# Kernel tuning notes

Measured on AMD Instinct MI355X. Metric: run time of the kernel, lower is better.

## Reference

```python
import jax, jax.numpy as jnp
import numpy as np

B, T, N, K = 8, 256, 128, 64
EPS = 1e-12  # torch.nn.functional.normalize clamp


def setup_inputs() -> dict:
    key = jax.random.key(0)
    ks = jax.random.split(key, 6)
    observation = jax.random.normal(ks[0], (B, T, K), dtype=jnp.float32)
    duration = jax.random.randint(ks[1], (B,), 1, T + 1)  # in [1, T]
    # time-varying transition matrices, strictly positive (probabilities pre-normalization)
    transition = jax.random.uniform(ks[2], (T, B, N, N), dtype=jnp.float32, minval=0.05, maxval=1.0)
    start_prob = jax.random.uniform(ks[3], (B, N), dtype=jnp.float32, minval=0.05, maxval=1.0)
    W_emit = jax.random.normal(ks[4], (K, N), dtype=jnp.float32) * 0.05
    b_emit = jnp.zeros((N,), dtype=jnp.float32)
    return {"observation": observation, "duration": duration, "transition": transition,
            "start_prob": start_prob, "W_emit": W_emit, "b_emit": b_emit}


def _log_emission(observation, W_emit, b_emit):
    # emission module: linear K->N then log-softmax over states -> [B,T,N]
    logits = jnp.einsum('btk,kn->btn', observation, W_emit) + b_emit
    return jax.nn.log_softmax(logits, axis=-1)


def reference(observation, duration, transition, start_prob, W_emit, b_emit):
    log_emit = _log_emission(observation, W_emit, b_emit)            # [B,T,N]
    # L1-normalize transitions along target dim (dim=2 of [B,N,N]) then log
    l1 = jnp.clip(jnp.sum(jnp.abs(transition), axis=-1, keepdims=True), EPS)
    logT = jnp.log(transition / l1)                                  # [T,B,N,N]

    la0 = log_emit[:, 0, :] + jnp.log(start_prob)                    # [B,N]

    def step(la_prev, xs):
        le_t, lT_t = xs                                              # [B,N], [B,N,N]
        # log-domain matmul: out[b,j] = logsumexp_k la_prev[b,k] + logT[b,k,j]
        la = le_t + jax.nn.logsumexp(la_prev[:, :, None] + lT_t, axis=1)
        return la, la

    le_seq = jnp.swapaxes(log_emit, 0, 1)                            # [T,B,N]
    _, alphas = jax.lax.scan(step, la0, (le_seq[1:], logT[1:]))      # [T-1,B,N]
    log_alpha = jnp.concatenate([la0[:, None, :], jnp.swapaxes(alphas, 0, 1)], axis=1)  # [B,T,N]

    log_sums = jax.nn.logsumexp(log_alpha, axis=2)                   # [B,T]
    log_probs = jnp.take_along_axis(log_sums, (duration - 1)[:, None], axis=1)  # [B,1]
    return log_probs
```

## Files before the change

### kernel.cpp

```cpp
#include <hip/hip_runtime.h>
#include <math.h>
#include <stdint.h>

#define B_ 8
#define T_ 256
#define N_ 128
#define K_ 64
#define NCH 32
#define LOG128 4.852030263919617f
#define STRIDE_S 4128

typedef __attribute__((ext_vector_type(2))) unsigned int u32x2;
typedef __attribute__((ext_vector_type(4))) unsigned int u32x4;
typedef __attribute__((ext_vector_type(4))) float f32x4;
typedef __attribute__((ext_vector_type(8))) short short8;

__device__ __forceinline__ uint32_t cvtpk(float lo, float hi) {
    uint32_t r;
    asm("v_cvt_pk_bf16_f32 %0, %1, %2" : "=v"(r) : "v"(lo), "v"(hi));
    return r;
}
__device__ __forceinline__ float blo(uint32_t w) { return __uint_as_float(w << 16); }
__device__ __forceinline__ float bhi(uint32_t w) { return __uint_as_float(w & 0xffff0000u); }

#define TRRD(dst, addr) asm volatile("ds_read_b64_tr_b16 %0, %1" : "=v"(dst) : "v"(addr) : "memory")
#define WAITL8  { asm volatile("s_waitcnt lgkmcnt(8)"  ::: "memory"); __builtin_amdgcn_sched_barrier(0); }
#define WAITL0  { asm volatile("s_waitcnt lgkmcnt(0)"  ::: "memory"); __builtin_amdgcn_sched_barrier(0); }

__global__ __launch_bounds__(128) void k_emit(
    const float* __restrict__ obs,
    const int*   __restrict__ dur,
    const float* __restrict__ W,
    const float* __restrict__ bias,
    float* __restrict__ e)
{
    int bt = blockIdx.x;
    int b  = bt >> 8;
    int t  = bt & 255;
    if (t >= dur[b]) return;
    int n = threadIdx.x;
    __shared__ float o[K_];
    __shared__ float wmax[2];
    __shared__ float wsum[2];
    if (n < K_) o[n] = obs[(size_t)bt * K_ + n];
    __syncthreads();
    float acc = bias[n];
    #pragma unroll
    for (int k = 0; k < K_; ++k)
        acc = fmaf(o[k], W[k * N_ + n], acc);
    float m = acc;
    #pragma unroll
    for (int off = 32; off; off >>= 1) m = fmaxf(m, __shfl_xor(m, off));
    int w = n >> 6;
    if ((n & 63) == 0) wmax[w] = m;
    __syncthreads();
    float M = fmaxf(wmax[0], wmax[1]);
    float ex = expf(acc - M);
    float s = ex;
    #pragma unroll
    for (int off = 32; off; off >>= 1) s += __shfl_xor(s, off);
    if ((n & 63) == 0) wsum[w] = s;
    __syncthreads();
    float S = wsum[0] + wsum[1];
    e[(size_t)bt * N_ + n] = ex / S;
}

__global__ __launch_bounds__(512, 1) void k_chunk(
    const float* __restrict__ trans,
    const int*   __restrict__ dur,
    const float* __restrict__ e,
    uint32_t* __restrict__ gout)
{
    const int bc = blockIdx.x;
    const int b  = bc & 7;
    const int c  = bc >> 3;
    const int d  = dur[b];
    const int t0 = c * 8 + 1;
    if (t0 > d - 1) return;
    int te = c * 8 + 8; if (te > d - 1) te = d - 1;

    const int tid  = threadIdx.x;
    const int lane = tid & 63;
    const int wv   = tid >> 6;
    const int cc   = lane & 15;
    const int gq   = lane >> 4;

    __shared__ __align__(16) uint8_t ldsC[2][8 * STRIDE_S];
    __shared__ __align__(16) uint8_t strips[8 * STRIDE_S];

    {
        uint32_t* sw = (uint32_t*)(strips + wv * STRIDE_S);
        #pragma unroll
        for (int i = 0; i < 16; ++i) sw[lane + i * 64] = 0;
        if (lane < 16)
            ((uint16_t*)(strips + wv * STRIDE_S))[(16 * wv + lane) * 16 + lane] = 0x3F80u;
    }

    const uint32_t sbase = (uint32_t)(uintptr_t)&strips[wv * STRIDE_S];
    const uint32_t lt    = (uint32_t)(cc * 2 + gq * 256);
    const int row0 = tid >> 5;
    const int jbp  = (tid & 31) >> 2;
    const int cc0  = (tid & 3) << 2;

    f32x4 acc[8];

    float4 v[8];
    float  ev[8];
    {
        const float4* gp = (const float4*)(trans + (((size_t)t0 * B_ + b) << 14));
        #pragma unroll
        for (int i = 0; i < 8; ++i) v[i] = gp[tid + i * 512];
        #pragma unroll
        for (int i = 0; i < 8; ++i)
            ev[i] = e[((size_t)b * T_ + (t0 - 1)) * N_ + row0 + i * 16];
    }

    int buf = 0;
    for (int t = t0; t <= te; ++t, buf ^= 1) {
        uint8_t* cb = ldsC[buf];
        const uint32_t cbase = (uint32_t)(uintptr_t)cb;

        #pragma unroll
        for (int i = 0; i < 8; ++i) {
            float ps = (v[i].x + v[i].y) + (v[i].z + v[i].w);
            ps += __shfl_xor(ps, 1);
            ps += __shfl_xor(ps, 2);
            ps += __shfl_xor(ps, 4);
            ps += __shfl_xor(ps, 8);
            ps += __shfl_xor(ps, 16);
            float sc = 128.0f * ev[i] / ps;
            uint32_t p0 = cvtpk(v[i].x * sc, v[i].y * sc);
            uint32_t p1 = cvtpk(v[i].z * sc, v[i].w * sc);
            *(uint2*)(cb + jbp * STRIDE_S + (row0 + i * 16) * 32 + cc0 * 2) = make_uint2(p0, p1);
        }

        if (t < te) {
            const float4* gp = (const float4*)(trans + (((size_t)(t + 1) * B_ + b) << 14));
            #pragma unroll
            for (int i = 0; i < 8; ++i) v[i] = gp[tid + i * 512];
            #pragma unroll
            for (int i = 0; i < 8; ++i)
                ev[i] = e[((size_t)b * T_ + t) * N_ + row0 + i * 16];
        }
        __syncthreads();

        u32x2 ra[8];
        #pragma unroll
        for (int kb = 0; kb < 4; ++kb) {
            uint32_t ad = sbase + (uint32_t)(kb * 1024) + lt;
            TRRD(ra[2 * kb],     ad);
            TRRD(ra[2 * kb + 1], ad + 128);
        }
        u32x2 rb[2][8];
#define ISSUE_B(S, JB) { \
        _Pragma("unroll") \
        for (int kb = 0; kb < 4; ++kb) { \
            uint32_t bd = cbase + (uint32_t)((JB) * STRIDE_S + kb * 1024) + lt; \
            TRRD(rb[S][2 * kb],     bd); \
            TRRD(rb[S][2 * kb + 1], bd + 128); } }
#define MFMA_JB(JB, S) { \
        f32x4 d4 = (f32x4){0.f, 0.f, 0.f, 0.f}; \
        _Pragma("unroll") \
        for (int kb = 0; kb < 4; ++kb) { \
            u32x4 tmp = (u32x4){rb[S][2 * kb].x, rb[S][2 * kb].y, rb[S][2 * kb + 1].x, rb[S][2 * kb + 1].y}; \
            short8 Bf = __builtin_bit_cast(short8, tmp); \
            d4 = __builtin_amdgcn_mfma_f32_16x16x32_bf16(A[kb], Bf, d4, 0, 0, 0); } \
        acc[JB] = d4; }

        ISSUE_B(0, 0);
        ISSUE_B(1, 1);
        WAITL8;
        short8 A[4];
        #pragma unroll
        for (int kb = 0; kb < 4; ++kb) {
            u32x4 tmp = (u32x4){ra[2 * kb].x, ra[2 * kb].y, ra[2 * kb + 1].x, ra[2 * kb + 1].y};
            A[kb] = __builtin_bit_cast(short8, tmp);
        }
        MFMA_JB(0, 0);
        ISSUE_B(0, 2); WAITL8; MFMA_JB(1, 1);
        ISSUE_B(1, 3); WAITL8; MFMA_JB(2, 0);
        ISSUE_B(0, 4); WAITL8; MFMA_JB(3, 1);
        ISSUE_B(1, 5); WAITL8; MFMA_JB(4, 0);
        ISSUE_B(0, 6); WAITL8; MFMA_JB(5, 1);
        ISSUE_B(1, 7); WAITL8; MFMA_JB(6, 0);
        WAITL0;                MFMA_JB(7, 1);
#undef ISSUE_B
#undef MFMA_JB

        #pragma unroll
        for (int jb = 0; jb < 8; ++jb) {
            uint32_t p0 = cvtpk(acc[jb][0], acc[jb][1]);
            uint32_t p1 = cvtpk(acc[jb][2], acc[jb][3]);
            *(uint2*)(strips + wv * STRIDE_S + (jb * 16 + cc) * 32 + gq * 8) = make_uint2(p0, p1);
        }
    }

    uint32_t* gdst = gout + ((size_t)(b * NCH + c) << 13);
    #pragma unroll
    for (int kb = 0; kb < 4; ++kb) {
        u32x2 e0, e1;
        uint32_t ad = sbase + (uint32_t)(kb * 1024) + lt;
        TRRD(e0, ad);
        TRRD(e1, ad + 128);
        WAITL0;
        u32x4 o = (u32x4){e0.x, e0.y, e1.x, e1.y};
        *(u32x4*)(gdst + (size_t)((16 * wv + cc) * 64 + kb * 16 + gq * 4)) = o;
    }
}

__global__ __launch_bounds__(256, 1) void k_comb(
    const uint32_t* __restrict__ gtiles,
    const int*   __restrict__ dur,
    const float* __restrict__ sp,
    const float* __restrict__ e,
    float* __restrict__ out)
{
    const int b   = blockIdx.x;
    const int tid = threadIdx.x;
    const int wv  = tid >> 6;
    const int l   = tid & 63;
    const int d   = dur[b];
    const int nc  = (d - 1 + 7) >> 3;

    __shared__ float  gl[2][N_];
    __shared__ float2 part[4][64];

    float g0 = sp[b * N_ + 2 * l];
    float g1 = sp[b * N_ + 2 * l + 1];
    float S  = -(float)(d - 1) * LOG128;
    if (tid < 64) *(float2*)&gl[0][2 * l] = make_float2(g0, g1);
    __syncthreads();

    const uint32_t* gb = gtiles + (((size_t)b * NCH) << 13) + l;
    uint32_t cwA[32], cwB[32];
    int p = 0;

#define LOADCH(P, C) { \
    const uint32_t* gp_ = gb + ((size_t)(C) << 13); \
    _Pragma("unroll") \
    for (int kk = 0; kk < 32; ++kk) P[kk] = gp_[(size_t)(wv * 32 + kk) * 64]; }

#define CSTEP(CUR, NXT) { \
    if (c + 1 < nc) LOADCH(NXT, c + 1); \
    float n0 = 0.f, n1 = 0.f; \
    _Pragma("unroll") \
    for (int kk = 0; kk < 32; ++kk) { \
        float gk = gl[p][wv * 32 + kk]; \
        n0 = fmaf(blo(CUR[kk]), gk, n0); \
        n1 = fmaf(bhi(CUR[kk]), gk, n1); } \
    part[wv][l] = make_float2(n0, n1); \
    __syncthreads(); \
    float2 q0 = part[0][l], q1 = part[1][l], q2 = part[2][l], q3 = part[3][l]; \
    float s0 = (q0.x + q1.x) + (q2.x + q3.x); \
    float s1 = (q0.y + q1.y) + (q2.y + q3.y); \
    float mx = fmaxf(s0, s1); \
    _Pragma("unroll") \
    for (int of = 1; of < 64; of <<= 1) mx = fmaxf(mx, __shfl_xor(mx, of)); \
    float mr = __builtin_amdgcn_rcpf(mx); \
    g0 = s0 * mr; g1 = s1 * mr; \
    S -= __logf(mr); \
    if (tid < 64) *(float2*)&gl[p ^ 1][2 * l] = make_float2(g0, g1); \
    __syncthreads(); \
    p ^= 1; \
}

    if (nc > 0) {
        LOADCH(cwA, 0);
        int c = 0;
        while (true) {
            CSTEP(cwA, cwB); ++c; if (c >= nc) break;
            CSTEP(cwB, cwA); ++c; if (c >= nc) break;
        }
    }
#undef LOADCH
#undef CSTEP

    float e0 = e[((size_t)b * T_ + (d - 1)) * N_ + 2 * l];
    float e1 = e[((size_t)b * T_ + (d - 1)) * N_ + 2 * l + 1];
    float sv = g0 * e0 + g1 * e1;
    #pragma unroll
    for (int of = 1; of < 64; of <<= 1) sv += __shfl_xor(sv, of);
    if (tid == 0) out[b] = S + logf(sv);
}

extern "C" void kernel_launch(void* const* d_in, const int* in_sizes, int n_in,
                              void* d_out, int out_size, void* d_ws, size_t ws_size,
                              hipStream_t stream) {
    const float* obs   = (const float*)d_in[0];
    const int*   dur   = (const int*)  d_in[1];
    const float* trans = (const float*)d_in[2];
    const float* sp    = (const float*)d_in[3];
    const float* W     = (const float*)d_in[4];
    const float* bias  = (const float*)d_in[5];
    float* out = (float*)d_out;

    float* e = (float*)d_ws;
    uint32_t* gout = (uint32_t*)((char*)d_ws + (size_t)B_ * T_ * N_ * 4);

    hipLaunchKernelGGL(k_emit,  dim3(B_ * T_),  dim3(128), 0, stream, obs, dur, W, bias, e);
    hipLaunchKernelGGL(k_chunk, dim3(B_ * NCH), dim3(512), 0, stream, trans, dur, e, gout);
    hipLaunchKernelGGL(k_comb,  dim3(B_),       dim3(256), 0, stream, gout, dur, sp, e, out);
}
```

Measured before the change: 70.17 us.

## Cut per-step barriers and deepen prefetch in the combine scan

The combine kernel now double-buffers the partial-sum array, so the second block barrier per step can go. Every wave writes the full normalized vector itself, so no wave has to wait to read another wave's writes. It adds a third register buffer so global loads are issued two chunks ahead, and splits the FMA accumulators to shorten the dependence chain. Both kernels use a barrier that waits only on LDS counters, not on outstanding global loads, so prefetches can stay in flight across the barrier. The costs are more register pressure and a reliance on waves writing identical shared values without racing.

```diff
diff --git a/kernel.cpp b/kernel.cpp
--- a/kernel.cpp
+++ b/kernel.cpp
@@ -26,6 +26,9 @@
 #define TRRD(dst, addr) asm volatile("ds_read_b64_tr_b16 %0, %1" : "=v"(dst) : "v"(addr) : "memory")
 #define WAITL8  { asm volatile("s_waitcnt lgkmcnt(8)"  ::: "memory"); __builtin_amdgcn_sched_barrier(0); }
 #define WAITL0  { asm volatile("s_waitcnt lgkmcnt(0)"  ::: "memory"); __builtin_amdgcn_sched_barrier(0); }
+#define BARRIER_LG() { asm volatile("s_waitcnt lgkmcnt(0)" ::: "memory"); \
+                       __builtin_amdgcn_s_barrier(); \
+                       __builtin_amdgcn_sched_barrier(0); }
 
 __global__ __launch_bounds__(128) void k_emit(
     const float* __restrict__ obs,
@@ -142,7 +145,7 @@
             for (int i = 0; i < 8; ++i)
                 ev[i] = e[((size_t)b * T_ + t) * N_ + row0 + i * 16];
         }
-        __syncthreads();
+        BARRIER_LG();
 
         u32x2 ra[8];
         #pragma unroll
@@ -223,16 +226,15 @@
     const int nc  = (d - 1 + 7) >> 3;
 
     __shared__ float  gl[2][N_];
-    __shared__ float2 part[4][64];
+    __shared__ float2 part[2][4][64];
 
     float g0 = sp[b * N_ + 2 * l];
     float g1 = sp[b * N_ + 2 * l + 1];
     float S  = -(float)(d - 1) * LOG128;
-    if (tid < 64) *(float2*)&gl[0][2 * l] = make_float2(g0, g1);
-    __syncthreads();
+    *(float2*)&gl[0][2 * l] = make_float2(g0, g1);
 
     const uint32_t* gb = gtiles + (((size_t)b * NCH) << 13) + l;
-    uint32_t cwA[32], cwB[32];
+    uint32_t cwA[32], cwB[32], cwC[32];
     int p = 0;
 
 #define LOADCH(P, C) { \
@@ -240,17 +242,20 @@
     _Pragma("unroll") \
     for (int kk = 0; kk < 32; ++kk) P[kk] = gp_[(size_t)(wv * 32 + kk) * 64]; }
 
-#define CSTEP(CUR, NXT) { \
-    if (c + 1 < nc) LOADCH(NXT, c + 1); \
-    float n0 = 0.f, n1 = 0.f; \
+#define CSTEP(CUR, NXT, CIDX) { \
+    if ((CIDX) + 2 < nc) LOADCH(NXT, (CIDX) + 2); \
+    float n0a = 0.f, n0b = 0.f, n1a = 0.f, n1b = 0.f; \
     _Pragma("unroll") \
-    for (int kk = 0; kk < 32; ++kk) { \
-        float gk = gl[p][wv * 32 + kk]; \
-        n0 = fmaf(blo(CUR[kk]), gk, n0); \
-        n1 = fmaf(bhi(CUR[kk]), gk, n1); } \
-    part[wv][l] = make_float2(n0, n1); \
-    __syncthreads(); \
-    float2 q0 = part[0][l], q1 = part[1][l], q2 = part[2][l], q3 = part[3][l]; \
+    for (int kk = 0; kk < 32; kk += 2) { \
+        float gk0 = gl[p][wv * 32 + kk]; \
+        float gk1 = gl[p][wv * 32 + kk + 1]; \
+        n0a = fmaf(blo(CUR[kk]),     gk0, n0a); \
+        n1a = fmaf(bhi(CUR[kk]),     gk0, n1a); \
+        n0b = fmaf(blo(CUR[kk + 1]), gk1, n0b); \
+        n1b = fmaf(bhi(CUR[kk + 1]), gk1, n1b); } \
+    part[p][wv][l] = make_float2(n0a + n0b, n1a + n1b); \
+    BARRIER_LG(); \
+    float2 q0 = part[p][0][l], q1 = part[p][1][l], q2 = part[p][2][l], q3 = part[p][3][l]; \
     float s0 = (q0.x + q1.x) + (q2.x + q3.x); \
     float s1 = (q0.y + q1.y) + (q2.y + q3.y); \
     float mx = fmaxf(s0, s1); \
@@ -259,17 +264,18 @@
     float mr = __builtin_amdgcn_rcpf(mx); \
     g0 = s0 * mr; g1 = s1 * mr; \
     S -= __logf(mr); \
-    if (tid < 64) *(float2*)&gl[p ^ 1][2 * l] = make_float2(g0, g1); \
-    __syncthreads(); \
+    *(float2*)&gl[p ^ 1][2 * l] = make_float2(g0, g1); \
     p ^= 1; \
 }
 
     if (nc > 0) {
         LOADCH(cwA, 0);
+        if (nc > 1) LOADCH(cwB, 1);
         int c = 0;
         while (true) {
-            CSTEP(cwA, cwB); ++c; if (c >= nc) break;
-            CSTEP(cwB, cwA); ++c; if (c >= nc) break;
+            CSTEP(cwA, cwC, c); ++c; if (c >= nc) break;
+            CSTEP(cwB, cwA, c); ++c; if (c >= nc) break;
+            CSTEP(cwC, cwB, c); ++c; if (c >= nc) break;
         }
     }
 #undef LOADCH
```

Measured after the change: 69.08 us. No clear change (-1.6%).
